# Optimization experiments

Measured on AMD Instinct MI355X. Metric: run time of the kernel, lower is better.

The kernel has to match this reference:

```python
import jax, jax.numpy as jnp
import numpy as np

B, S, DMODEL, NHEAD = 2, 2048, 1024, 16
DK = DMODEL // NHEAD
INITRANGE = 0.1


def setup_inputs() -> dict:
    key = jax.random.key(0)
    kq, kk, kv, kwq, kwk, kwv, kwo = jax.random.split(key, 7)
    unif = lambda k, shape: jax.random.uniform(k, shape, jnp.float32, -INITRANGE, INITRANGE)
    return {
        "Q": jax.random.normal(kq, (B, S, DMODEL), jnp.float32),
        "K": jax.random.normal(kk, (B, S, DMODEL), jnp.float32),
        "V": jax.random.normal(kv, (B, S, DMODEL), jnp.float32),
        "WQ": unif(kwq, (NHEAD, DMODEL, DK)),
        "WK": unif(kwk, (NHEAD, DMODEL, DK)),
        "WV": unif(kwv, (NHEAD, DMODEL, DK)),
        "WO": unif(kwo, (NHEAD * DK, DMODEL)),
    }


def reference(Q, K, V, WQ, WK, WV, WO):
    dk = WQ.shape[-1]
    # per-head projections: [B,S,D] x [H,D,dk] -> [B,H,S,dk]
    Qi = jnp.einsum('bsd,hdk->bhsk', Q, WQ)
    Ki = jnp.einsum('bsd,hdk->bhsk', K, WK)
    Vi = jnp.einsum('bsd,hdk->bhsk', V, WV)
    scale = 1.0 / jnp.sqrt(jnp.asarray(dk, Qi.dtype))
    # full attention matrix [B,H,S,S] (faithful to the hand-rolled module; dropout in eval mode)
    attn = jax.nn.softmax(jnp.einsum('bhsk,bhtk->bhst', Qi, Ki) * scale, axis=-1)
    headi = jnp.einsum('bhst,bhtk->bhsk', attn, Vi)  # [B,H,S,dk]
    b, h, s, _ = headi.shape
    # NOTE: original does a raw reshape of contiguous (B,H,S,dk) -> (B,S,H*dk),
    # which mixes head and sequence axes in memory order. jnp row-major reshape
    # reproduces exactly the same element layout.
    out = headi.reshape(b, s, h * dk) @ WO  # [B,S,DMODEL]
    return out
```

## Files before the change

### kernel.cpp

```cpp
#include <hip/hip_runtime.h>
#include <hip/hip_bf16.h>
#include <stdint.h>

typedef unsigned short u16;
typedef unsigned int u32;
typedef __attribute__((ext_vector_type(4))) float f32x4;
typedef __attribute__((ext_vector_type(16))) float f32x16;
typedef __attribute__((ext_vector_type(8))) short bf16x8;
typedef __attribute__((ext_vector_type(4))) unsigned int u32x4;
typedef __attribute__((ext_vector_type(2))) unsigned int u32x2;

#define DEV __device__ __forceinline__

DEV u16 f2bf(float f) {
  union { float f; uint32_t u; } v; v.f = f;
  uint32_t u = v.u;
  return (u16)((u + 0x7fffu + ((u >> 16) & 1u)) >> 16);
}
DEV float bf2f(u16 h) {
  union { uint32_t u; float f; } v; v.u = ((uint32_t)h) << 16;
  return v.f;
}

DEV u32 cvtpk(float a, float b) {
  u32 r;
  asm("v_cvt_pk_bf16_f32 %0, %1, %2" : "=v"(r) : "v"(a), "v"(b));
  return r;
}

DEV void plswap(u32& a, u32& b) {
  asm("v_permlane32_swap_b32 %0, %1" : "+v"(a), "+v"(b));
}

DEV float fexp2(float x) {
  float r;
  asm("v_exp_f32 %0, %1" : "=v"(r) : "v"(x));
  return r;
}

DEV void gload_lds16(const u16* g, u16* l) {
  __builtin_amdgcn_global_load_lds(
      (const __attribute__((address_space(1))) void*)g,
      (__attribute__((address_space(3))) void*)l, 16, 0, 0);
}

__global__ __launch_bounds__(256) void prep_tw_kernel(
    const float* __restrict__ Q, const float* __restrict__ K, const float* __restrict__ V,
    const float* __restrict__ WQ, const float* __restrict__ WK, const float* __restrict__ WV,
    const float* __restrict__ WO,
    u16* __restrict__ Qb, u16* __restrict__ Kb, u16* __restrict__ Vb,
    u16* __restrict__ Wt, u16* __restrict__ Wot) {
  __shared__ __align__(16) u16 tl[64][72];
  const int tid = threadIdx.x;
  if (blockIdx.x < 4096) {
    const int i = blockIdx.x * 256 + tid;
#pragma unroll
    for (int it = 0; it < 3; ++it) {
      int idx = it * 1048576 + i;
      int which = idx >> 20, j = idx & 1048575;
      const float* src = which == 0 ? Q : (which == 1 ? K : V);
      u16* dst = which == 0 ? Qb : (which == 1 ? Kb : Vb);
      float4 v = ((const float4*)src)[j];
      u32x2 pk;
      pk[0] = (u32)f2bf(v.x) | ((u32)f2bf(v.y) << 16);
      pk[1] = (u32)f2bf(v.z) | ((u32)f2bf(v.w) << 16);
      *(u32x2*)(dst + (size_t)j * 4) = pk;
    }
    return;
  }
  const int bid = blockIdx.x - 4096;
  const float* src;
  u16* dst;
  int rstride;
  if (bid < 768) {
    int p = bid >> 8, rest = bid & 255;
    int h = rest >> 4, dt = rest & 15;
    const float* W = p == 0 ? WQ : (p == 1 ? WK : WV);
    src = W + (size_t)(h * 1024 + dt * 64) * 64;
    dst = Wt + (size_t)p * 1048576 + (size_t)h * 64 * 1024 + dt * 64;
    rstride = 64;
  } else {
    int idx2 = bid - 768;
    int kt = idx2 >> 4, ct = idx2 & 15;
    src = WO + (size_t)kt * 64 * 1024 + ct * 64;
    dst = Wot + (size_t)ct * 64 * 1024 + kt * 64;
    rstride = 1024;
  }
#pragma unroll
  for (int i = 0; i < 2; ++i) {
    int idx = i * 256 + tid;
    int row = idx >> 3, c8 = idx & 7;
    const float* sp = src + (size_t)row * rstride + c8 * 8;
    float4 a = *(const float4*)sp;
    float4 b = *(const float4*)(sp + 4);
    u32x4 pk;
    pk[0] = (u32)f2bf(a.x) | ((u32)f2bf(a.y) << 16);
    pk[1] = (u32)f2bf(a.z) | ((u32)f2bf(a.w) << 16);
    pk[2] = (u32)f2bf(b.x) | ((u32)f2bf(b.y) << 16);
    pk[3] = (u32)f2bf(b.z) | ((u32)f2bf(b.w) << 16);
    *(u32x4*)&tl[row][c8 * 8] = pk;
  }
  __syncthreads();
#pragma unroll
  for (int i = 0; i < 2; ++i) {
    int idx = i * 256 + tid;
    int row2 = idx >> 3, s8 = idx & 7;
    u32x4 outv;
    u16* tp = (u16*)&outv;
#pragma unroll
    for (int j = 0; j < 8; ++j) tp[j] = tl[s8 * 8 + j][row2];
    *(u32x4*)(dst + (size_t)row2 * 1024 + s8 * 8) = outv;
  }
}

__global__ __launch_bounds__(256, 3) void gemm_proj_kernel(const u16* __restrict__ A,
                                                           const u16* __restrict__ Bt,
                                                           u16* __restrict__ Cout,
                                                           u16* __restrict__ VtOut) {
  __shared__ __align__(16) u16 Alds[128 * 64];
  __shared__ __align__(16) u16 Blds[128 * 64];
  const size_t zo = blockIdx.z;
  A += zo * 4194304;
  Bt += zo * 1048576;
  const int tid = threadIdx.x;
  const int l = tid & 63, w = tid >> 6;
  const int wm = w >> 1, wn = w & 1;
  const int d = blockIdx.x + 32 * blockIdx.y;
  const int orig = (d & 7) * 32 + (d >> 3);
  const int tileM = (orig & 31) * 128, tileN = (orig >> 5) * 128;
  const int lr = l >> 3, lch = l & 7;

  f32x4 acc[4][4] = {};

  for (int kt = 0; kt < 16; ++kt) {
    const int k0 = kt * 64;
#pragma unroll
    for (int i = 0; i < 4; ++i) {
      int r = i * 32 + w * 8 + lr;
      int sch = lch ^ (r & 7);
      gload_lds16(A + (size_t)(tileM + r) * 1024 + k0 + sch * 8, Alds + i * 2048 + w * 512);
      gload_lds16(Bt + (size_t)(tileN + r) * 1024 + k0 + sch * 8, Blds + i * 2048 + w * 512);
    }
    __syncthreads();
    bf16x8 af[4][2], bfr[4][2];
#pragma unroll
    for (int m = 0; m < 4; ++m) {
#pragma unroll
      for (int kk = 0; kk < 2; ++kk) {
        int row = wm * 64 + m * 16 + (l & 15);
        int ch = ((l >> 4) + kk * 4) ^ (row & 7);
        af[m][kk] = *(const bf16x8*)(Alds + row * 64 + ch * 8);
        int rowb = wn * 64 + m * 16 + (l & 15);
        int chb = ((l >> 4) + kk * 4) ^ (rowb & 7);
        bfr[m][kk] = *(const bf16x8*)(Blds + rowb * 64 + chb * 8);
      }
    }
#pragma unroll
    for (int m = 0; m < 4; ++m)
#pragma unroll
      for (int n = 0; n < 4; ++n)
#pragma unroll
        for (int kk = 0; kk < 2; ++kk)
          acc[m][n] = __builtin_amdgcn_mfma_f32_16x16x32_bf16(af[m][kk], bfr[n][kk], acc[m][n], 0, 0, 0);
    __syncthreads();
  }
#pragma unroll
  for (int m = 0; m < 4; ++m) {
    int row0 = tileM + wm * 64 + m * 16 + ((l >> 4) << 2);
#pragma unroll
    for (int n = 0; n < 4; ++n) {
      int col = tileN + wn * 64 + n * 16 + (l & 15);
#pragma unroll
      for (int q = 0; q < 4; ++q) {
        u16 val = f2bf(acc[m][n][q]);
        if (zo == 2) {
          int g = row0 + q;
          int bq = g >> 11, s = g & 2047;
          int hh = col >> 6, dk = col & 63;
          VtOut[((((size_t)bq << 4) + hh) * 64 + dk) * 2048 + s] = val;
        } else {
          Cout[zo * 4194304 + (size_t)(row0 + q) * 1024 + col] = val;
        }
      }
    }
  }
}

__global__ __launch_bounds__(256, 4) void gemm_out_kernel(const u16* __restrict__ A,
                                                          const u16* __restrict__ Bt,
                                                          float* __restrict__ Cout) {
  __shared__ __align__(16) u16 Alds[64 * 64];
  __shared__ __align__(16) u16 Blds[128 * 64];
  const int tid = threadIdx.x;
  const int l = tid & 63, w = tid >> 6;
  const int wm = w >> 1, wn = w & 1;
  const int d = blockIdx.x;
  const int orig = (d & 7) * 64 + (d >> 3);
  const int tileM = (orig >> 3) * 64, tileN = (orig & 7) * 128;
  const int lr = l >> 3, lch = l & 7;

  f32x4 acc[2][4] = {};

  for (int kt = 0; kt < 16; ++kt) {
    const int k0 = kt * 64;
#pragma unroll
    for (int i = 0; i < 2; ++i) {
      int r = i * 32 + w * 8 + lr;
      int sch = lch ^ (r & 7);
      gload_lds16(A + (size_t)(tileM + r) * 1024 + k0 + sch * 8, Alds + i * 2048 + w * 512);
    }
#pragma unroll
    for (int i = 0; i < 4; ++i) {
      int r = i * 32 + w * 8 + lr;
      int sch = lch ^ (r & 7);
      gload_lds16(Bt + (size_t)(tileN + r) * 1024 + k0 + sch * 8, Blds + i * 2048 + w * 512);
    }
    __syncthreads();
    bf16x8 af[2][2], bfr[4][2];
#pragma unroll
    for (int m = 0; m < 2; ++m)
#pragma unroll
      for (int kk = 0; kk < 2; ++kk) {
        int row = wm * 32 + m * 16 + (l & 15);
        int ch = ((l >> 4) + kk * 4) ^ (row & 7);
        af[m][kk] = *(const bf16x8*)(Alds + row * 64 + ch * 8);
      }
#pragma unroll
    for (int n = 0; n < 4; ++n)
#pragma unroll
      for (int kk = 0; kk < 2; ++kk) {
        int rowb = wn * 64 + n * 16 + (l & 15);
        int chb = ((l >> 4) + kk * 4) ^ (rowb & 7);
        bfr[n][kk] = *(const bf16x8*)(Blds + rowb * 64 + chb * 8);
      }
#pragma unroll
    for (int m = 0; m < 2; ++m)
#pragma unroll
      for (int n = 0; n < 4; ++n)
#pragma unroll
        for (int kk = 0; kk < 2; ++kk)
          acc[m][n] = __builtin_amdgcn_mfma_f32_16x16x32_bf16(af[m][kk], bfr[n][kk], acc[m][n], 0, 0, 0);
    __syncthreads();
  }
#pragma unroll
  for (int m = 0; m < 2; ++m) {
    int row0 = tileM + wm * 32 + m * 16 + ((l >> 4) << 2);
#pragma unroll
    for (int n = 0; n < 4; ++n) {
      int col = tileN + wn * 64 + n * 16 + (l & 15);
#pragma unroll
      for (int q = 0; q < 4; ++q)
        Cout[(size_t)(row0 + q) * 1024 + col] = acc[m][n][q];
    }
  }
}

__global__ __launch_bounds__(256, 4) void attn_kernel(const u16* __restrict__ Qi,
                                                      const u16* __restrict__ Ki,
                                                      const u16* __restrict__ Vt,
                                                      u16* __restrict__ Op,
                                                      float* __restrict__ Lp) {
  __shared__ __align__(16) u16 Kl[2][4096];
  __shared__ __align__(16) u16 Vl[2][4096];
  const int tid = threadIdx.x;
  const int l = tid & 63, w = tid >> 6;
  const int lq = l & 31, hi = l >> 5;
  const int lr = l >> 3, lch = l & 7;
  const int dd = blockIdx.x;
  const int orig = (dd & 7) * 128 + (dd >> 3);
  const int bh = orig >> 5;
  const int rem = orig & 31;
  const int qb = rem >> 1, kvh = rem & 1;
  const int b = bh >> 4, h = bh & 15;
  const int qt = qb * 128 + w * 32;
  const int tb = kvh * 1024;

  const u16* Kbase = Ki + (size_t)b * 2048 * 1024 + h * 64;
  const u16* Vbase = Vt + (size_t)bh * 64 * 2048;

  bf16x8 qf[4];
  {
    const u16* qp = Qi + (size_t)(b * 2048 + qt + lq) * 1024 + h * 64 + hi * 8;
#pragma unroll
    for (int s = 0; s < 4; ++s) {
      u32x4 t4 = *(const u32x4*)(qp + s * 16);
      u16* tp = (u16*)&t4;
#pragma unroll
      for (int j = 0; j < 8; ++j) tp[j] = f2bf(bf2f(tp[j]) * 0.1803368867f);
      qf[s] = *(bf16x8*)&t4;
    }
  }

  f32x16 o0 = {}, o1 = {};
  float l_r = 0.f;

  auto STAGE = [&](int bb, int t) {
#pragma unroll
    for (int i = 0; i < 2; ++i) {
      int r = i * 32 + w * 8 + lr;
      int sch = lch ^ (r & 7);
      gload_lds16(Kbase + (size_t)(tb + t * 64 + r) * 1024 + sch * 8,
                  Kl[bb] + i * 2048 + w * 512);
      gload_lds16(Vbase + (size_t)r * 2048 + tb + t * 64 + sch * 8,
                  Vl[bb] + i * 2048 + w * 512);
    }
  };

  STAGE(0, 0);

#pragma unroll 2
  for (int tile = 0; tile < 16; ++tile) {
    const int cur = tile & 1;
    __syncthreads();
    if (tile + 1 < 16) STAGE(cur ^ 1, tile + 1);
    const u16* kl = Kl[cur];
    const u16* vl = Vl[cur];

    f32x16 s0 = {}, s1 = {};
    __builtin_amdgcn_s_setprio(1);
#pragma unroll
    for (int s = 0; s < 4; ++s) {
      int row = lq, c = s * 2 + hi;
      bf16x8 kf = *(const bf16x8*)(kl + row * 64 + (c ^ (row & 7)) * 8);
      s0 = __builtin_amdgcn_mfma_f32_32x32x16_bf16(kf, qf[s], s0, 0, 0, 0);
    }
#pragma unroll
    for (int s = 0; s < 4; ++s) {
      int row = 32 + lq, c = s * 2 + hi;
      bf16x8 kf = *(const bf16x8*)(kl + row * 64 + (c ^ (row & 7)) * 8);
      s1 = __builtin_amdgcn_mfma_f32_32x32x16_bf16(kf, qf[s], s1, 0, 0, 0);
    }
    __builtin_amdgcn_s_setprio(0);

    float rs = 0.f;
    bf16x8 pa[4];
#pragma unroll
    for (int s4 = 0; s4 < 4; ++s4) {
      const int rb = 8 * (s4 & 1);
      float p[8];
#pragma unroll
      for (int j = 0; j < 8; ++j) {
        float sv = (s4 < 2) ? ((const float*)&s0)[rb + j] : ((const float*)&s1)[rb + j];
        p[j] = fexp2(sv);
      }
      rs += ((p[0] + p[1]) + (p[2] + p[3])) + ((p[4] + p[5]) + (p[6] + p[7]));
      u32 w10 = cvtpk(p[0], p[1]);
      u32 w11 = cvtpk(p[2], p[3]);
      u32 w20 = cvtpk(p[4], p[5]);
      u32 w21 = cvtpk(p[6], p[7]);
      plswap(w10, w20);
      plswap(w11, w21);
      u32x4 af;
      af[0] = w10;
      af[1] = w11;
      af[2] = w20;
      af[3] = w21;
      pa[s4] = *(bf16x8*)&af;
    }
    rs += __shfl_xor(rs, 32, 64);
    l_r += rs;

    __builtin_amdgcn_s_setprio(1);
#pragma unroll
    for (int s4 = 0; s4 < 4; ++s4) {
      int rowd = lq, c = s4 * 2 + hi;
      bf16x8 vf = *(const bf16x8*)(vl + rowd * 64 + (c ^ (rowd & 7)) * 8);
      o0 = __builtin_amdgcn_mfma_f32_32x32x16_bf16(pa[s4], vf, o0, 0, 0, 0);
    }
#pragma unroll
    for (int s4 = 0; s4 < 4; ++s4) {
      int rowd = 32 + lq, c = s4 * 2 + hi;
      bf16x8 vf = *(const bf16x8*)(vl + rowd * 64 + (c ^ (rowd & 7)) * 8);
      o1 = __builtin_amdgcn_mfma_f32_32x32x16_bf16(pa[s4], vf, o1, 0, 0, 0);
    }
    __builtin_amdgcn_s_setprio(0);
  }

#pragma unroll
  for (int r = 0; r < 16; ++r) {
    int qr = (r & 3) + 8 * (r >> 2) + 4 * hi;
    u16* hp = Op + (size_t)kvh * 4194304 + ((size_t)bh * 2048 + qt + qr) * 64;
    hp[lq] = f2bf(o0[r]);
    hp[32 + lq] = f2bf(o1[r]);
  }
  if (hi == 0) Lp[(size_t)kvh * 65536 + (size_t)bh * 2048 + qt + lq] = l_r;
}

__global__ __launch_bounds__(256) void combine_kernel(const u16* __restrict__ Op,
                                                      const float* __restrict__ Lp,
                                                      u16* __restrict__ Hd) {
  const int idx = blockIdx.x * 256 + threadIdx.x;
  const int g = idx >> 3, j = idx & 7;
  const float fac = 1.f / (Lp[g] + Lp[65536 + g]);
  const size_t off = (size_t)g * 64 + j * 8;
  u32x4 va = *(const u32x4*)(Op + off);
  u32x4 vb = *(const u32x4*)(Op + 4194304 + off);
  const u16* pa = (const u16*)&va;
  const u16* pb = (const u16*)&vb;
  u32x4 outv;
  u16* po = (u16*)&outv;
#pragma unroll
  for (int e = 0; e < 8; ++e) po[e] = f2bf((bf2f(pa[e]) + bf2f(pb[e])) * fac);
  *(u32x4*)(Hd + off) = outv;
}

extern "C" void kernel_launch(void* const* d_in, const int* in_sizes, int n_in,
                              void* d_out, int out_size, void* d_ws, size_t ws_size,
                              hipStream_t stream) {
  const float* Q = (const float*)d_in[0];
  const float* K = (const float*)d_in[1];
  const float* V = (const float*)d_in[2];
  const float* WQ = (const float*)d_in[3];
  const float* WK = (const float*)d_in[4];
  const float* WV = (const float*)d_in[5];
  const float* WO = (const float*)d_in[6];
  float* out = (float*)d_out;

  size_t off = 0;
  char* ws = (char*)d_ws;
  auto nxt = [&](size_t n) { void* p = ws + off; off += (n + 255) & ~(size_t)255; return p; };
  u16* Qb = (u16*)nxt(3ull * 4096 * 1024 * 2);
  u16* Qi = (u16*)nxt(3ull * 4096 * 1024 * 2);
  u16* Vtb = (u16*)nxt(4096ull * 1024 * 2);
  u16* Hd = (u16*)nxt(4096ull * 1024 * 2);
  u16* Wt = (u16*)nxt(3ull * 1048576 * 2);
  u16* Wot = (u16*)nxt(1048576ull * 2);
  float* Lp = (float*)nxt(2ull * 65536 * 4);
  u16* Ki = Qi + 4194304;
  u16* Op = Qb;

  prep_tw_kernel<<<5120, 256, 0, stream>>>(Q, K, V, WQ, WK, WV, WO, Qb, Qb + 4194304,
                                           Qb + 2 * 4194304, Wt, Wot);

  gemm_proj_kernel<<<dim3(32, 8, 3), 256, 0, stream>>>(Qb, Wt, Qi, Vtb);

  attn_kernel<<<1024, 256, 0, stream>>>(Qi, Ki, Vtb, Op, Lp);

  combine_kernel<<<2048, 256, 0, stream>>>(Op, Lp, Hd);

  gemm_out_kernel<<<512, 256, 0, stream>>>(Hd, Wot, out);
}
```

Baseline: 128.5 us.

## Fuse fp32-to-bf16 activation conversion into projection GEMM A-tile loads

Drops the separate pass that converts Q/K/V from fp32 to bf16. The projection GEMM now streams fp32 activations straight into LDS with a swizzled layout and converts them to bf16 while building MFMA fragments. This removes a full read and write of the activations and one kernel's worth of work. In exchange the GEMM loads twice the bytes per A tile, uses 32KB of LDS for A, and adds conversion instructions to the inner loop, which may hurt occupancy and LDS bandwidth.

New measurement: 145.3 us. 1.13x slower.

```diff
diff --git a/kernel.cpp b/kernel.cpp
--- a/kernel.cpp
+++ b/kernel.cpp
@@ -43,32 +43,18 @@
       (const __attribute__((address_space(1))) void*)g,
       (__attribute__((address_space(3))) void*)l, 16, 0, 0);
 }
-
-__global__ __launch_bounds__(256) void prep_tw_kernel(
-    const float* __restrict__ Q, const float* __restrict__ K, const float* __restrict__ V,
+DEV void gload_lds16f(const float* g, float* l) {
+  __builtin_amdgcn_global_load_lds(
+      (const __attribute__((address_space(1))) void*)g,
+      (__attribute__((address_space(3))) void*)l, 16, 0, 0);
+}
+
+__global__ __launch_bounds__(256) void transposeW_kernel(
     const float* __restrict__ WQ, const float* __restrict__ WK, const float* __restrict__ WV,
-    const float* __restrict__ WO,
-    u16* __restrict__ Qb, u16* __restrict__ Kb, u16* __restrict__ Vb,
-    u16* __restrict__ Wt, u16* __restrict__ Wot) {
+    const float* __restrict__ WO, u16* __restrict__ Wt, u16* __restrict__ Wot) {
   __shared__ __align__(16) u16 tl[64][72];
   const int tid = threadIdx.x;
-  if (blockIdx.x < 4096) {
-    const int i = blockIdx.x * 256 + tid;
-#pragma unroll
-    for (int it = 0; it < 3; ++it) {
-      int idx = it * 1048576 + i;
-      int which = idx >> 20, j = idx & 1048575;
-      const float* src = which == 0 ? Q : (which == 1 ? K : V);
-      u16* dst = which == 0 ? Qb : (which == 1 ? Kb : Vb);
-      float4 v = ((const float4*)src)[j];
-      u32x2 pk;
-      pk[0] = (u32)f2bf(v.x) | ((u32)f2bf(v.y) << 16);
-      pk[1] = (u32)f2bf(v.z) | ((u32)f2bf(v.w) << 16);
-      *(u32x2*)(dst + (size_t)j * 4) = pk;
-    }
-    return;
-  }
-  const int bid = blockIdx.x - 4096;
+  const int bid = blockIdx.x;
   const float* src;
   u16* dst;
   int rstride;
@@ -94,10 +80,10 @@
     float4 a = *(const float4*)sp;
     float4 b = *(const float4*)(sp + 4);
     u32x4 pk;
-    pk[0] = (u32)f2bf(a.x) | ((u32)f2bf(a.y) << 16);
-    pk[1] = (u32)f2bf(a.z) | ((u32)f2bf(a.w) << 16);
-    pk[2] = (u32)f2bf(b.x) | ((u32)f2bf(b.y) << 16);
-    pk[3] = (u32)f2bf(b.z) | ((u32)f2bf(b.w) << 16);
+    pk[0] = cvtpk(a.x, a.y);
+    pk[1] = cvtpk(a.z, a.w);
+    pk[2] = cvtpk(b.x, b.y);
+    pk[3] = cvtpk(b.z, b.w);
     *(u32x4*)&tl[row][c8 * 8] = pk;
   }
   __syncthreads();
@@ -113,17 +99,17 @@
   }
 }
 
-__global__ __launch_bounds__(256, 3) void gemm_proj_kernel(const u16* __restrict__ A,
-                                                           const u16* __restrict__ Bt,
-                                                           u16* __restrict__ Cout,
-                                                           u16* __restrict__ VtOut) {
-  __shared__ __align__(16) u16 Alds[128 * 64];
+__global__ __launch_bounds__(256, 3) void gemm_proj_kernel(
+    const float* __restrict__ F0, const float* __restrict__ F1, const float* __restrict__ F2,
+    const u16* __restrict__ Bt, u16* __restrict__ Cout, u16* __restrict__ VtOut) {
+  __shared__ __align__(16) float Afl[128 * 64];
   __shared__ __align__(16) u16 Blds[128 * 64];
   const size_t zo = blockIdx.z;
-  A += zo * 4194304;
+  const float* Af = zo == 0 ? F0 : (zo == 1 ? F1 : F2);
   Bt += zo * 1048576;
   const int tid = threadIdx.x;
   const int l = tid & 63, w = tid >> 6;
+  const int x = l & 15, g = l >> 4;
   const int wm = w >> 1, wn = w & 1;
   const int d = blockIdx.x + 32 * blockIdx.y;
   const int orig = (d & 7) * 32 + (d >> 3);
@@ -135,10 +121,16 @@
   for (int kt = 0; kt < 16; ++kt) {
     const int k0 = kt * 64;
 #pragma unroll
+    for (int i = 0; i < 8; ++i) {
+      int row = i * 16 + w * 4 + g;
+      int sch = x ^ (row & 15);
+      gload_lds16f(Af + (size_t)(tileM + row) * 1024 + k0 + sch * 4,
+                   Afl + i * 1024 + w * 256);
+    }
+#pragma unroll
     for (int i = 0; i < 4; ++i) {
       int r = i * 32 + w * 8 + lr;
       int sch = lch ^ (r & 7);
-      gload_lds16(A + (size_t)(tileM + r) * 1024 + k0 + sch * 8, Alds + i * 2048 + w * 512);
       gload_lds16(Bt + (size_t)(tileN + r) * 1024 + k0 + sch * 8, Blds + i * 2048 + w * 512);
     }
     __syncthreads();
@@ -147,11 +139,19 @@
     for (int m = 0; m < 4; ++m) {
 #pragma unroll
       for (int kk = 0; kk < 2; ++kk) {
-        int row = wm * 64 + m * 16 + (l & 15);
-        int ch = ((l >> 4) + kk * 4) ^ (row & 7);
-        af[m][kk] = *(const bf16x8*)(Alds + row * 64 + ch * 8);
-        int rowb = wn * 64 + m * 16 + (l & 15);
-        int chb = ((l >> 4) + kk * 4) ^ (rowb & 7);
+        int row = wm * 64 + m * 16 + x;
+        int c0 = 2 * (g + kk * 4);
+        int p0 = c0 ^ x;
+        f32x4 a = *(const f32x4*)(Afl + row * 64 + p0 * 4);
+        f32x4 b = *(const f32x4*)(Afl + row * 64 + (p0 ^ 1) * 4);
+        u32x4 pk;
+        pk[0] = cvtpk(a[0], a[1]);
+        pk[1] = cvtpk(a[2], a[3]);
+        pk[2] = cvtpk(b[0], b[1]);
+        pk[3] = cvtpk(b[2], b[3]);
+        af[m][kk] = *(bf16x8*)&pk;
+        int rowb = wn * 64 + m * 16 + x;
+        int chb = (g + kk * 4) ^ (rowb & 7);
         bfr[m][kk] = *(const bf16x8*)(Blds + rowb * 64 + chb * 8);
       }
     }
@@ -166,16 +166,16 @@
   }
 #pragma unroll
   for (int m = 0; m < 4; ++m) {
-    int row0 = tileM + wm * 64 + m * 16 + ((l >> 4) << 2);
+    int row0 = tileM + wm * 64 + m * 16 + (g << 2);
 #pragma unroll
     for (int n = 0; n < 4; ++n) {
-      int col = tileN + wn * 64 + n * 16 + (l & 15);
+      int col = tileN + wn * 64 + n * 16 + x;
 #pragma unroll
       for (int q = 0; q < 4; ++q) {
         u16 val = f2bf(acc[m][n][q]);
         if (zo == 2) {
-          int g = row0 + q;
-          int bq = g >> 11, s = g & 2047;
+          int gg = row0 + q;
+          int bq = gg >> 11, s = gg & 2047;
           int hh = col >> 6, dk = col & 63;
           VtOut[((((size_t)bq << 4) + hh) * 64 + dk) * 2048 + s] = val;
         } else {
@@ -419,20 +419,18 @@
   size_t off = 0;
   char* ws = (char*)d_ws;
   auto nxt = [&](size_t n) { void* p = ws + off; off += (n + 255) & ~(size_t)255; return p; };
-  u16* Qb = (u16*)nxt(3ull * 4096 * 1024 * 2);
   u16* Qi = (u16*)nxt(3ull * 4096 * 1024 * 2);
   u16* Vtb = (u16*)nxt(4096ull * 1024 * 2);
   u16* Hd = (u16*)nxt(4096ull * 1024 * 2);
   u16* Wt = (u16*)nxt(3ull * 1048576 * 2);
   u16* Wot = (u16*)nxt(1048576ull * 2);
   float* Lp = (float*)nxt(2ull * 65536 * 4);
+  u16* Op = (u16*)nxt(2ull * 4194304 * 2);
   u16* Ki = Qi + 4194304;
-  u16* Op = Qb;
-
-  prep_tw_kernel<<<5120, 256, 0, stream>>>(Q, K, V, WQ, WK, WV, WO, Qb, Qb + 4194304,
-                                           Qb + 2 * 4194304, Wt, Wot);
-
-  gemm_proj_kernel<<<dim3(32, 8, 3), 256, 0, stream>>>(Qb, Wt, Qi, Vtb);
+
+  transposeW_kernel<<<1024, 256, 0, stream>>>(WQ, WK, WV, WO, Wt, Wot);
+
+  gemm_proj_kernel<<<dim3(32, 8, 3), 256, 0, stream>>>(Q, K, V, Wt, Qi, Vtb);
 
   attn_kernel<<<1024, 256, 0, stream>>>(Qi, Ki, Vtb, Op, Lp);
 
```
